# Kernel tuning notes

Measured on AMD Instinct MI355X. Metric: run time of the kernel, lower is better.

The kernel has to match this reference:

```python
import jax, jax.numpy as jnp
import numpy as np
import math

B, S, D, H = 2, 2048, 1024, 16
DH = D // H
DFF = 4 * D
EPS = 1e-6


def layer_norm(x, g, b):
    # Faithful to the torch module: std is Bessel-corrected (ddof=1) and eps is
    # added to std (not variance).
    mean = jnp.mean(x, axis=-1, keepdims=True)
    var = jnp.sum((x - mean) ** 2, axis=-1, keepdims=True) / (x.shape[-1] - 1)
    return g * (x - mean) / (jnp.sqrt(var) + EPS) + b


def gelu_tanh(h):
    c = math.sqrt(2.0 / math.pi)
    return 0.5 * h * (1.0 + jnp.tanh(c * (h + 0.044715 * h ** 3)))


def attention(x, mask, wq, bq, wk, bk, wv, bv, wo, bo):
    b, s, d = x.shape
    q = (x @ wq + bq).reshape(b, s, H, DH)
    k = (x @ wk + bk).reshape(b, s, H, DH)
    v = (x @ wv + bv).reshape(b, s, H, DH)
    corr = jnp.einsum('bqhd,bkhd->bhqk', q, k) / math.sqrt(DH)  # [B,H,S,S]
    # original builds mask[:,None,:].repeat -> key-axis padding mask
    corr = jnp.where(mask[:, None, None, :] == 0, jnp.float32(-1e9), corr)
    prob = jax.nn.softmax(corr, axis=-1)
    hid = jnp.einsum('bhqk,bkhd->bqhd', prob, v).reshape(b, s, d)
    return hid @ wo + bo


def setup_inputs() -> dict:
    key = jax.random.key(0)
    ks = jax.random.split(key, 16)
    std = 0.02
    inp = {
        'hidden': jax.random.normal(ks[0], (B, S, D), jnp.float32),
        'mask': jax.random.randint(ks[1], (B, S), 0, 2, jnp.int32),
        'wq': jax.random.normal(ks[2], (D, D), jnp.float32) * std,
        'bq': jnp.zeros((D,), jnp.float32),
        'wk': jax.random.normal(ks[3], (D, D), jnp.float32) * std,
        'bk': jnp.zeros((D,), jnp.float32),
        'wv': jax.random.normal(ks[4], (D, D), jnp.float32) * std,
        'bv': jnp.zeros((D,), jnp.float32),
        'wo': jax.random.normal(ks[5], (D, D), jnp.float32) * std,
        'bo': jnp.zeros((D,), jnp.float32),
        'w1': jax.random.normal(ks[6], (D, DFF), jnp.float32) * std,
        'b1': jnp.zeros((DFF,), jnp.float32),
        'w2': jax.random.normal(ks[7], (DFF, D), jnp.float32) * std,
        'b2': jnp.zeros((D,), jnp.float32),
        'ln1_g': jnp.ones((D,), jnp.float32),
        'ln1_b': jnp.zeros((D,), jnp.float32),
        'ln2_g': jnp.ones((D,), jnp.float32),
        'ln2_b': jnp.zeros((D,), jnp.float32),
    }
    return inp


def reference(hidden, mask, wq, bq, wk, bk, wv, bv, wo, bo, w1, b1, w2, b2,
              ln1_g, ln1_b, ln2_g, ln2_b):
    # pre-norm residual attention sublayer (dropout = identity in eval)
    h = hidden + attention(layer_norm(hidden, ln1_g, ln1_b), mask,
                           wq, bq, wk, bk, wv, bv, wo, bo)
    # pre-norm residual FFN sublayer with tanh-GELU
    ff_in = layer_norm(h, ln2_g, ln2_b)
    h = h + (gelu_tanh(ff_in @ w1 + b1) @ w2 + b2)
    return h
```

## Files before the change

### kernel.cpp

```cpp
#include <hip/hip_runtime.h>

#define BB 2
#define SS 2048
#define DD 1024
#define HH 16
#define DHH 64
#define DFF 4096
#define MM (BB * SS)

typedef unsigned short u16;
typedef short short8 __attribute__((ext_vector_type(8)));
typedef float f32x4 __attribute__((ext_vector_type(4)));

__device__ __forceinline__ float b2f(u16 u) {
    return __uint_as_float(((unsigned)u) << 16);
}
__device__ __forceinline__ u16 f2b(float f) {
    unsigned u = __float_as_uint(f);
    unsigned r = (u + 0x7fffu + ((u >> 16) & 1u)) >> 16;
    return (u16)r;
}
__device__ __forceinline__ float gelu_tanh_f(float x) {
    float x3 = x * x * x;
    float t = 0.7978845608028654f * (x + 0.044715f * x3);
    return 0.5f * x * (1.0f + tanhf(t));
}
__device__ __forceinline__ void cp16(const u16* g, u16* l) {
    __builtin_amdgcn_global_load_lds(
        (const __attribute__((address_space(1))) void*)g,
        (__attribute__((address_space(3))) void*)l, 16, 0, 0);
}

__global__ __launch_bounds__(256) void wconv(const float* __restrict__ W,
                                             u16* __restrict__ WT,
                                             int Kdim, int Ndim) {
    __shared__ float tile[64][65];
    const int t = threadIdx.x;
    const int k0 = blockIdx.x * 64, n0 = blockIdx.y * 64;
    const int c = t & 63, r0 = (t >> 6) * 16;
#pragma unroll
    for (int i = 0; i < 16; ++i)
        tile[r0 + i][c] = W[(size_t)(k0 + r0 + i) * Ndim + n0 + c];
    __syncthreads();
    const int k4 = (t & 15) * 4, nr = t >> 4;
#pragma unroll
    for (int i = 0; i < 4; ++i) {
        int n = nr + 16 * i;
        ushort4 u = {f2b(tile[k4 + 0][n]), f2b(tile[k4 + 1][n]),
                     f2b(tile[k4 + 2][n]), f2b(tile[k4 + 3][n])};
        *(ushort4*)&WT[(size_t)(n0 + n) * Kdim + k0 + k4] = u;
    }
}

__global__ __launch_bounds__(256) void pack3(const float* __restrict__ a,
                                             const float* __restrict__ b,
                                             const float* __restrict__ c,
                                             float* __restrict__ o) {
    int i = blockIdx.x * 256 + threadIdx.x;
    o[i] = (i < 1024) ? a[i] : ((i < 2048) ? b[i - 1024] : c[i - 2048]);
}

template <typename TI>
__global__ __launch_bounds__(256) void ln_kernel(const TI* __restrict__ x,
                                                 const float* __restrict__ g,
                                                 const float* __restrict__ bb,
                                                 u16* __restrict__ out) {
    __shared__ float red[8];
    const int row = blockIdx.x;
    const int t = threadIdx.x;
    const size_t base = (size_t)row * DD;

    float xv[4];
#pragma unroll
    for (int i = 0; i < 4; ++i) {
        int j = t + i * 256;
        if constexpr (sizeof(TI) == 2) xv[i] = b2f(((const u16*)x)[base + j]);
        else                            xv[i] = ((const float*)x)[base + j];
    }

    float part = xv[0] + xv[1] + xv[2] + xv[3];
#pragma unroll
    for (int off = 32; off > 0; off >>= 1) part += __shfl_xor(part, off);
    if ((t & 63) == 0) red[t >> 6] = part;
    __syncthreads();
    const float mean = (red[0] + red[1] + red[2] + red[3]) * (1.0f / 1024.0f);

    float dv[4];
#pragma unroll
    for (int i = 0; i < 4; ++i) dv[i] = xv[i] - mean;
    float p2 = dv[0] * dv[0] + dv[1] * dv[1] + dv[2] * dv[2] + dv[3] * dv[3];
#pragma unroll
    for (int off = 32; off > 0; off >>= 1) p2 += __shfl_xor(p2, off);
    if ((t & 63) == 0) red[4 + (t >> 6)] = p2;
    __syncthreads();
    const float var = (red[4] + red[5] + red[6] + red[7]) * (1.0f / 1023.0f);
    const float rden = 1.0f / (sqrtf(var) + 1e-6f);

#pragma unroll
    for (int i = 0; i < 4; ++i) {
        int j = t + i * 256;
        out[base + j] = f2b(g[j] * dv[i] * rden + bb[j]);
    }
}

template <int EPI>
__device__ __forceinline__ void gemm_store(int row, int col, float v,
                                           const void* res, void* out, int Ndim) {
    if (EPI == 0 || EPI == 4) {
        if (EPI == 4) v *= 0.125f;
        const int bq = row >> 11, ss = row & 2047;
        const int hh = col >> 6, dh = col & 63;
        ((u16*)out)[(((size_t)bq * HH + hh) * SS + ss) * DHH + dh] = f2b(v);
    } else if (EPI == 5) {
        const int reg = col >> 10, cc = col & 1023;
        if (reg == 0) v *= 0.125f;
        const int bq = row >> 11, ss = row & 2047;
        const int hh = cc >> 6, dh = cc & 63;
        ((u16*)out)[(size_t)reg * 4194304 +
                    (((size_t)bq * HH + hh) * SS + ss) * DHH + dh] = f2b(v);
    } else if (EPI == 1) {
        const size_t o = (size_t)row * Ndim + col;
        ((u16*)out)[o] = f2b(v + ((const float*)res)[o]);
    } else if (EPI == 2) {
        ((u16*)out)[(size_t)row * Ndim + col] = f2b(gelu_tanh_f(v));
    } else {
        const size_t o = (size_t)row * Ndim + col;
        ((float*)out)[o] = v + b2f(((const u16*)res)[o]);
    }
}

template <int EPI, int TM>
__global__ __launch_bounds__(256) void gemm_as(const u16* __restrict__ A,
                                               const u16* __restrict__ BTg,
                                               const float* __restrict__ bias,
                                               const void* __restrict__ res,
                                               void* __restrict__ out,
                                               int Ndim, int Kdim) {
    constexpr int NI = (TM == 128) ? 4 : 2;
    constexpr int NCA = TM / 32;
    __shared__ __align__(16) u16 As[TM * 64];
    __shared__ __align__(16) u16 Bs[128 * 64];

    const int t = threadIdx.x;
    const int w = t >> 6, l = t & 63;
    const int lm = l & 15, lg = l >> 4;
    const int m0 = blockIdx.y * TM, n0 = blockIdx.x * 128;
    const int wro = (TM == 128) ? (w >> 1) * 64 : 0;
    const int wco = (TM == 128) ? (w & 1) * 64 : w * 32;

    f32x4 acc[4][NI];
#pragma unroll
    for (int mi = 0; mi < 4; ++mi)
#pragma unroll
        for (int ni = 0; ni < NI; ++ni) acc[mi][ni] = (f32x4){0.f, 0.f, 0.f, 0.f};

    for (int k0 = 0; k0 < Kdim; k0 += 64) {
#pragma unroll
        for (int j = 0; j < NCA; ++j) {
            const int c = (w * NCA + j) * 64 + l;
            const int r = c >> 3, g = (c & 7) ^ (r & 7);
            cp16(A + (size_t)(m0 + r) * Kdim + k0 + g * 8,
                 &As[(w * NCA + j) * 512]);
        }
#pragma unroll
        for (int j = 0; j < 4; ++j) {
            const int c = (w * 4 + j) * 64 + l;
            const int r = c >> 3, g = (c & 7) ^ (r & 7);
            cp16(BTg + (size_t)(n0 + r) * Kdim + k0 + g * 8,
                 &Bs[(w * 4 + j) * 512]);
        }
        __syncthreads();

#pragma unroll
        for (int ks = 0; ks < 64; ks += 32) {
            short8 af[4], bf[NI];
#pragma unroll
            for (int mi = 0; mi < 4; ++mi) {
                const int row = wro + mi * 16 + lm;
                af[mi] = *(const short8*)&As[row * 64 + ((ks + lg * 8) ^ ((row & 7) * 8))];
            }
#pragma unroll
            for (int ni = 0; ni < NI; ++ni) {
                const int nn = wco + ni * 16 + lm;
                bf[ni] = *(const short8*)&Bs[nn * 64 + ((ks + lg * 8) ^ ((nn & 7) * 8))];
            }
#pragma unroll
            for (int mi = 0; mi < 4; ++mi)
#pragma unroll
                for (int ni = 0; ni < NI; ++ni)
                    acc[mi][ni] = __builtin_amdgcn_mfma_f32_16x16x32_bf16(
                        af[mi], bf[ni], acc[mi][ni], 0, 0, 0);
        }
        __syncthreads();
    }

#pragma unroll
    for (int ni = 0; ni < NI; ++ni) {
        const int col = n0 + wco + ni * 16 + lm;
        const float bv = bias[col];
#pragma unroll
        for (int mi = 0; mi < 4; ++mi)
#pragma unroll
            for (int r = 0; r < 4; ++r)
                gemm_store<EPI>(m0 + wro + mi * 16 + lg * 4 + r, col,
                                acc[mi][ni][r] + bv, res, out, Ndim);
    }
}

template <int EPI, int TM>
__global__ __launch_bounds__(256) void gemm_fb(const u16* __restrict__ A,
                                               const float* __restrict__ W,
                                               const float* __restrict__ bias,
                                               const void* __restrict__ res,
                                               void* __restrict__ out,
                                               int Ndim, int Kdim) {
    constexpr int NI = (TM == 128) ? 4 : 2;
    __shared__ __align__(16) u16 As[TM * 64];
    __shared__ __align__(16) u16 BT[128 * 64];

    const int t = threadIdx.x;
    const int w = t >> 6, l = t & 63;
    const int lm = l & 15, lg = l >> 4;
    const int m0 = blockIdx.y * TM, n0 = blockIdx.x * 128;
    const int wro = (TM == 128) ? (w >> 1) * 64 : 0;
    const int wco = (TM == 128) ? (w & 1) * 64 : w * 32;

    f32x4 acc[4][NI];
#pragma unroll
    for (int mi = 0; mi < 4; ++mi)
#pragma unroll
        for (int ni = 0; ni < NI; ++ni) acc[mi][ni] = (f32x4){0.f, 0.f, 0.f, 0.f};

    const int bn = t & 127;
    const int bk4 = (t >> 7) * 4;

    for (int k0 = 0; k0 < Kdim; k0 += 64) {
#pragma unroll
        for (int it = 0; it < TM / 32; ++it) {
            int idx = it * 256 + t;
            int row = idx >> 3, c8 = (idx & 7) * 8;
            short8 v = *(const short8*)(A + (size_t)(m0 + row) * Kdim + k0 + c8);
            *(short8*)&As[row * 64 + (c8 ^ ((row & 7) * 8))] = v;
        }
#pragma unroll
        for (int it = 0; it < 8; ++it) {
            int kq = it * 8 + bk4;
            const float* wp = W + (size_t)(k0 + kq) * Ndim + n0 + bn;
            ushort4 u = {f2b(wp[0]), f2b(wp[(size_t)Ndim]),
                         f2b(wp[2 * (size_t)Ndim]), f2b(wp[3 * (size_t)Ndim])};
            *(ushort4*)&BT[bn * 64 + (kq ^ ((bn & 7) * 8))] = u;
        }
        __syncthreads();

#pragma unroll
        for (int ks = 0; ks < 64; ks += 32) {
            short8 af[4], bf[NI];
#pragma unroll
            for (int mi = 0; mi < 4; ++mi) {
                const int row = wro + mi * 16 + lm;
                af[mi] = *(const short8*)&As[row * 64 + ((ks + lg * 8) ^ ((row & 7) * 8))];
            }
#pragma unroll
            for (int ni = 0; ni < NI; ++ni) {
                const int nn = wco + ni * 16 + lm;
                bf[ni] = *(const short8*)&BT[nn * 64 + ((ks + lg * 8) ^ ((nn & 7) * 8))];
            }
#pragma unroll
            for (int mi = 0; mi < 4; ++mi)
#pragma unroll
                for (int ni = 0; ni < NI; ++ni)
                    acc[mi][ni] = __builtin_amdgcn_mfma_f32_16x16x32_bf16(
                        af[mi], bf[ni], acc[mi][ni], 0, 0, 0);
        }
        __syncthreads();
    }

#pragma unroll
    for (int ni = 0; ni < NI; ++ni) {
        const int col = n0 + wco + ni * 16 + lm;
        const float bv = bias[col];
#pragma unroll
        for (int mi = 0; mi < 4; ++mi)
#pragma unroll
            for (int r = 0; r < 4; ++r)
                gemm_store<EPI>(m0 + wro + mi * 16 + lg * 4 + r, col,
                                acc[mi][ni][r] + bv, res, out, Ndim);
    }
}

__global__ __launch_bounds__(256) void attn_mfma2(const u16* __restrict__ qg,
                                                  const u16* __restrict__ kg,
                                                  const u16* __restrict__ vg,
                                                  const int* __restrict__ mask,
                                                  u16* __restrict__ hid) {
    __shared__ __align__(16) u16 Ks[64 * 72];
    __shared__ __align__(16) u16 VTs[64 * 72];
    __shared__ __align__(16) float maskf[64];

    const int t = threadIdx.x;
    const int w = t >> 6;
    const int l = t & 63;
    const int lm = l & 15, lg = l >> 4;
    const int h = blockIdx.y, b = blockIdx.z;
    const int qbase = blockIdx.x * 128 + w * 32;
    const size_t bhS = ((size_t)b * HH + h) * SS;

    short8 qlo[2], qhi[2];
#pragma unroll
    for (int qp = 0; qp < 2; ++qp) {
        const u16* qrow = qg + (bhS + qbase + qp * 16 + lm) * DHH + lg * 8;
        qlo[qp] = *(const short8*)qrow;
        qhi[qp] = *(const short8*)(qrow + 32);
    }

    f32x4 acc[2][4];
#pragma unroll
    for (int qp = 0; qp < 2; ++qp)
#pragma unroll
        for (int i = 0; i < 4; ++i) acc[qp][i] = (f32x4){0.f, 0.f, 0.f, 0.f};
    float sume[2] = {0.f, 0.f};

    const int kq = (t & 15) * 4, dq = (t >> 4) * 4;

    for (int kt = 0; kt < SS; kt += 64) {
        __syncthreads();
#pragma unroll
        for (int it = 0; it < 4; ++it) {
            int idx = it * 256 + t;
            int row = idx >> 4, c4 = (idx & 15) * 4;
            ushort4 u = *(const ushort4*)(kg + (bhS + kt + row) * DHH + c4);
            *(ushort4*)&Ks[row * 72 + c4] = u;
        }
        {
            ushort4 a0 = *(const ushort4*)(vg + (bhS + kt + kq + 0) * DHH + dq);
            ushort4 a1 = *(const ushort4*)(vg + (bhS + kt + kq + 1) * DHH + dq);
            ushort4 a2 = *(const ushort4*)(vg + (bhS + kt + kq + 2) * DHH + dq);
            ushort4 a3 = *(const ushort4*)(vg + (bhS + kt + kq + 3) * DHH + dq);
            ushort4 w0 = {a0.x, a1.x, a2.x, a3.x};
            ushort4 w1 = {a0.y, a1.y, a2.y, a3.y};
            ushort4 w2 = {a0.z, a1.z, a2.z, a3.z};
            ushort4 w3 = {a0.w, a1.w, a2.w, a3.w};
            *(ushort4*)&VTs[(dq + 0) * 72 + kq] = w0;
            *(ushort4*)&VTs[(dq + 1) * 72 + kq] = w1;
            *(ushort4*)&VTs[(dq + 2) * 72 + kq] = w2;
            *(ushort4*)&VTs[(dq + 3) * 72 + kq] = w3;
        }
        if (t < 64) maskf[t] = mask[b * SS + kt + t] ? 1.0f : 0.0f;
        __syncthreads();

#pragma unroll
        for (int kb = 0; kb < 64; kb += 32) {
            short8 kfa[2], kfc[2];
#pragma unroll
            for (int s = 0; s < 2; ++s) {
                const int keyrow = kb + 8 * (lm >> 2) + 4 * s + (lm & 3);
                const u16* kr = &Ks[keyrow * 72 + lg * 8];
                kfa[s] = *(const short8*)kr;
                kfc[s] = *(const short8*)(kr + 32);
            }
            short8 p8[2];
#pragma unroll
            for (int qp = 0; qp < 2; ++qp) {
                float ev[8];
#pragma unroll
                for (int s = 0; s < 2; ++s) {
                    f32x4 c = (f32x4){0.f, 0.f, 0.f, 0.f};
                    c = __builtin_amdgcn_mfma_f32_16x16x32_bf16(kfa[s], qlo[qp], c, 0, 0, 0);
                    c = __builtin_amdgcn_mfma_f32_16x16x32_bf16(kfc[s], qhi[qp], c, 0, 0, 0);
                    const float4 mv = *(const float4*)&maskf[kb + 8 * lg + 4 * s];
                    float e0 = __expf(c[0]) * mv.x;
                    float e1 = __expf(c[1]) * mv.y;
                    float e2 = __expf(c[2]) * mv.z;
                    float e3 = __expf(c[3]) * mv.w;
                    sume[qp] += e0 + e1 + e2 + e3;
                    ev[4 * s + 0] = e0; ev[4 * s + 1] = e1;
                    ev[4 * s + 2] = e2; ev[4 * s + 3] = e3;
                }
#pragma unroll
                for (int i = 0; i < 8; ++i)
                    p8[qp][i] = (short)(__float_as_uint(ev[i]) >> 16);
            }
#pragma unroll
            for (int d0 = 0; d0 < 4; ++d0) {
                const short8 v8 = *(const short8*)&VTs[(d0 * 16 + lm) * 72 + kb + lg * 8];
#pragma unroll
                for (int qp = 0; qp < 2; ++qp)
                    acc[qp][d0] = __builtin_amdgcn_mfma_f32_16x16x32_bf16(
                        p8[qp], v8, acc[qp][d0], 0, 0, 0);
            }
        }
    }

#pragma unroll
    for (int qp = 0; qp < 2; ++qp) {
        float s = sume[qp];
        s += __shfl_xor(s, 16);
        s += __shfl_xor(s, 32);
        float rinv[4];
#pragma unroll
        for (int r = 0; r < 4; ++r) rinv[r] = 1.0f / __shfl(s, 4 * lg + r);
#pragma unroll
        for (int d0 = 0; d0 < 4; ++d0)
#pragma unroll
            for (int r = 0; r < 4; ++r) {
                const int q = qbase + qp * 16 + 4 * lg + r;
                hid[(size_t)(b * SS + q) * DD + h * DHH + d0 * 16 + lm] =
                    f2b(acc[qp][d0][r] * rinv[r]);
            }
    }
}

extern "C" void kernel_launch(void* const* d_in, const int* in_sizes, int n_in,
                              void* d_out, int out_size, void* d_ws, size_t ws_size,
                              hipStream_t stream) {
    (void)in_sizes; (void)n_in; (void)out_size;

    const float* hidden = (const float*)d_in[0];
    const int*   mask   = (const int*)d_in[1];
    const float* wq = (const float*)d_in[2];  const float* bq = (const float*)d_in[3];
    const float* wk = (const float*)d_in[4];  const float* bk = (const float*)d_in[5];
    const float* wv = (const float*)d_in[6];  const float* bv = (const float*)d_in[7];
    const float* wo = (const float*)d_in[8];  const float* bo = (const float*)d_in[9];
    const float* w1 = (const float*)d_in[10]; const float* b1 = (const float*)d_in[11];
    const float* w2 = (const float*)d_in[12]; const float* b2 = (const float*)d_in[13];
    const float* ln1g = (const float*)d_in[14]; const float* ln1b = (const float*)d_in[15];
    const float* ln2g = (const float*)d_in[16]; const float* ln2b = (const float*)d_in[17];

    char* ws = (char*)d_ws;
    u16* R0 = (u16*)(ws + 0);
    u16* R1 = (u16*)(ws + 8388608);
    u16* R2 = (u16*)(ws + 16777216);
    u16* R3 = (u16*)(ws + 25165824);
    float* outp = (float*)d_out;

    const size_t WTOFF = 33554432;
    const bool big = ws_size >= WTOFF + 25165824 + 16384;

    if (big) {
        u16* qkvT = (u16*)(ws + WTOFF);
        u16* woT  = (u16*)(ws + WTOFF + 6291456);
        u16* w1T  = (u16*)(ws + WTOFF + 8388608);
        u16* w2T  = (u16*)(ws + WTOFF + 16777216);
        float* bqkv = (float*)(ws + WTOFF + 25165824);

        wconv<<<dim3(DD / 64, DD / 64), 256, 0, stream>>>(wq, qkvT, DD, DD);
        wconv<<<dim3(DD / 64, DD / 64), 256, 0, stream>>>(wk, qkvT + (size_t)1024 * DD, DD, DD);
        wconv<<<dim3(DD / 64, DD / 64), 256, 0, stream>>>(wv, qkvT + (size_t)2048 * DD, DD, DD);
        wconv<<<dim3(DD / 64, DD / 64), 256, 0, stream>>>(wo, woT, DD, DD);
        wconv<<<dim3(DD / 64, DFF / 64), 256, 0, stream>>>(w1, w1T, DD, DFF);
        wconv<<<dim3(DFF / 64, DD / 64), 256, 0, stream>>>(w2, w2T, DFF, DD);
        pack3<<<12, 256, 0, stream>>>(bq, bk, bv, bqkv);

        ln_kernel<float><<<MM, 256, 0, stream>>>(hidden, ln1g, ln1b, R0);
        gemm_as<5, 128><<<dim3(3072 / 128, MM / 128), 256, 0, stream>>>(
            R0, qkvT, bqkv, nullptr, R1, 3072, DD);
        attn_mfma2<<<dim3(SS / 128, HH, BB), 256, 0, stream>>>(R1, R2, R3, mask, R0);
        gemm_as<1, 128><<<dim3(DD / 128, MM / 128), 256, 0, stream>>>(
            R0, woT, bo, hidden, R3, DD, DD);
        ln_kernel<u16><<<MM, 256, 0, stream>>>(R3, ln2g, ln2b, R0);
        for (int s2 = 0; s2 < 2; ++s2) {
            const size_t r0 = (size_t)s2 * 2048;
            gemm_as<2, 128><<<dim3(DFF / 128, 2048 / 128), 256, 0, stream>>>(
                R0 + r0 * DD, w1T, b1, nullptr, R1, DFF, DD);
            gemm_as<3, 64><<<dim3(DD / 128, 2048 / 64), 256, 0, stream>>>(
                R1, w2T, b2, R3 + r0 * DD, outp + r0 * DD, DD, DFF);
        }
    } else {
        ln_kernel<float><<<MM, 256, 0, stream>>>(hidden, ln1g, ln1b, R0);
        gemm_fb<4, 128><<<dim3(DD / 128, MM / 128), 256, 0, stream>>>(R0, wq, bq, nullptr, R1, DD, DD);
        gemm_fb<0, 128><<<dim3(DD / 128, MM / 128), 256, 0, stream>>>(R0, wk, bk, nullptr, R2, DD, DD);
        gemm_fb<0, 128><<<dim3(DD / 128, MM / 128), 256, 0, stream>>>(R0, wv, bv, nullptr, R3, DD, DD);
        attn_mfma2<<<dim3(SS / 128, HH, BB), 256, 0, stream>>>(R1, R2, R3, mask, R0);
        gemm_fb<1, 128><<<dim3(DD / 128, MM / 128), 256, 0, stream>>>(R0, wo, bo, hidden, R3, DD, DD);
        ln_kernel<u16><<<MM, 256, 0, stream>>>(R3, ln2g, ln2b, R0);
        for (int s2 = 0; s2 < 2; ++s2) {
            const size_t r0 = (size_t)s2 * 2048;
            gemm_fb<2, 128><<<dim3(DFF / 128, 2048 / 128), 256, 0, stream>>>(
                R0 + r0 * DD, w1, b1, nullptr, R1, DFF, DD);
            gemm_fb<3, 64><<<dim3(DD / 128, 2048 / 64), 256, 0, stream>>>(
                R1, w2, b2, R3 + r0 * DD, outp + r0 * DD, DD, DFF);
        }
    }
}
```

Measured before the change: 491.3 us.

## Split attention over key halves with merge kernel, batch weight conversions

Attention is split along the key dimension into two halves, doubling the grid so more workgroups can fill the GPU. Each half writes unnormalized bf16 partial outputs and per-row exp sums, and a new merge kernel adds the two partials and divides by the total sum. The six weight-conversion launches are merged into two kernels, and the second one runs after attention so its output buffer can hold the attention partials first. This adds extra global traffic for the partials, an extra bf16 rounding of the unnormalized values, and reuses the output buffer as scratch space.

```diff
diff --git a/kernel.cpp b/kernel.cpp
--- a/kernel.cpp
+++ b/kernel.cpp
@@ -31,12 +31,11 @@
         (__attribute__((address_space(3))) void*)l, 16, 0, 0);
 }
 
-__global__ __launch_bounds__(256) void wconv(const float* __restrict__ W,
-                                             u16* __restrict__ WT,
-                                             int Kdim, int Ndim) {
-    __shared__ float tile[64][65];
-    const int t = threadIdx.x;
-    const int k0 = blockIdx.x * 64, n0 = blockIdx.y * 64;
+__device__ __forceinline__ void wconv_tile(const float* __restrict__ W,
+                                           u16* __restrict__ WT,
+                                           int Kdim, int Ndim, int gk, int gn,
+                                           float (*tile)[65], int t) {
+    const int k0 = gk * 64, n0 = gn * 64;
     const int c = t & 63, r0 = (t >> 6) * 16;
 #pragma unroll
     for (int i = 0; i < 16; ++i)
@@ -49,6 +48,38 @@
         ushort4 u = {f2b(tile[k4 + 0][n]), f2b(tile[k4 + 1][n]),
                      f2b(tile[k4 + 2][n]), f2b(tile[k4 + 3][n])};
         *(ushort4*)&WT[(size_t)(n0 + n) * Kdim + k0 + k4] = u;
+    }
+}
+
+__global__ __launch_bounds__(256) void wconvA(const float* __restrict__ wq,
+                                              const float* __restrict__ wk,
+                                              const float* __restrict__ wv,
+                                              const float* __restrict__ w2,
+                                              u16* __restrict__ qkvT,
+                                              u16* __restrict__ w2T) {
+    __shared__ float tile[64][65];
+    const int bid = blockIdx.x, t = threadIdx.x;
+    if (bid < 768) {
+        const int r = bid >> 8, li = bid & 255;
+        const float* W = (r == 0) ? wq : ((r == 1) ? wk : wv);
+        wconv_tile(W, qkvT + (size_t)r * 1048576, DD, DD, li & 15, li >> 4, tile, t);
+    } else {
+        const int li = bid - 768;
+        wconv_tile(w2, w2T, DFF, DD, li & 63, li >> 6, tile, t);
+    }
+}
+
+__global__ __launch_bounds__(256) void wconvB(const float* __restrict__ wo,
+                                              const float* __restrict__ w1,
+                                              u16* __restrict__ woT,
+                                              u16* __restrict__ w1T) {
+    __shared__ float tile[64][65];
+    const int bid = blockIdx.x, t = threadIdx.x;
+    if (bid < 256) {
+        wconv_tile(wo, woT, DD, DD, bid & 15, bid >> 4, tile, t);
+    } else {
+        const int li = bid - 256;
+        wconv_tile(w1, w1T, DD, DFF, li & 15, li >> 4, tile, t);
     }
 }
 
@@ -288,11 +319,13 @@
     }
 }
 
-__global__ __launch_bounds__(256) void attn_mfma2(const u16* __restrict__ qg,
+__global__ __launch_bounds__(256) void attn_split(const u16* __restrict__ qg,
                                                   const u16* __restrict__ kg,
                                                   const u16* __restrict__ vg,
                                                   const int* __restrict__ mask,
-                                                  u16* __restrict__ hid) {
+                                                  u16* __restrict__ p0,
+                                                  u16* __restrict__ p1,
+                                                  float* __restrict__ sume_g) {
     __shared__ __align__(16) u16 Ks[64 * 72];
     __shared__ __align__(16) u16 VTs[64 * 72];
     __shared__ __align__(16) float maskf[64];
@@ -301,9 +334,13 @@
     const int w = t >> 6;
     const int l = t & 63;
     const int lm = l & 15, lg = l >> 4;
-    const int h = blockIdx.y, b = blockIdx.z;
+    const int h = blockIdx.y;
+    const int z = blockIdx.z;
+    const int b = z >> 1, half = z & 1;
     const int qbase = blockIdx.x * 128 + w * 32;
     const size_t bhS = ((size_t)b * HH + h) * SS;
+    u16* pO = half ? p1 : p0;
+    const int kt0 = half * (SS / 2);
 
     short8 qlo[2], qhi[2];
 #pragma unroll
@@ -322,7 +359,7 @@
 
     const int kq = (t & 15) * 4, dq = (t >> 4) * 4;
 
-    for (int kt = 0; kt < SS; kt += 64) {
+    for (int kt = kt0; kt < kt0 + SS / 2; kt += 64) {
         __syncthreads();
 #pragma unroll
         for (int it = 0; it < 4; ++it) {
@@ -396,6 +433,144 @@
         float s = sume[qp];
         s += __shfl_xor(s, 16);
         s += __shfl_xor(s, 32);
+        if (l < 16)
+            sume_g[(size_t)half * (BB * HH * SS) + bhS + qbase + qp * 16 + lm] = s;
+#pragma unroll
+        for (int d0 = 0; d0 < 4; ++d0)
+#pragma unroll
+            for (int r = 0; r < 4; ++r) {
+                const int q = qbase + qp * 16 + 4 * lg + r;
+                pO[(size_t)(b * SS + q) * DD + h * DHH + d0 * 16 + lm] =
+                    f2b(acc[qp][d0][r]);
+            }
+    }
+}
+
+__global__ __launch_bounds__(256) void attn_merge(const u16* __restrict__ p1,
+                                                  const float* __restrict__ sume_g,
+                                                  u16* __restrict__ hid) {
+    const int row = blockIdx.x;
+    const int b = row >> 11, s = row & 2047;
+    const int t = threadIdx.x;
+#pragma unroll
+    for (int i = 0; i < 4; ++i) {
+        const int j = t + i * 256;
+        const int h = j >> 6;
+        const size_t si = ((size_t)b * HH + h) * SS + s;
+        const float d = sume_g[si] + sume_g[(size_t)BB * HH * SS + si];
+        const size_t o = (size_t)row * DD + j;
+        hid[o] = f2b((b2f(hid[o]) + b2f(p1[o])) / d);
+    }
+}
+
+__global__ __launch_bounds__(256) void attn_mfma2(const u16* __restrict__ qg,
+                                                  const u16* __restrict__ kg,
+                                                  const u16* __restrict__ vg,
+                                                  const int* __restrict__ mask,
+                                                  u16* __restrict__ hid) {
+    __shared__ __align__(16) u16 Ks[64 * 72];
+    __shared__ __align__(16) u16 VTs[64 * 72];
+    __shared__ __align__(16) float maskf[64];
+
+    const int t = threadIdx.x;
+    const int w = t >> 6;
+    const int l = t & 63;
+    const int lm = l & 15, lg = l >> 4;
+    const int h = blockIdx.y, b = blockIdx.z;
+    const int qbase = blockIdx.x * 128 + w * 32;
+    const size_t bhS = ((size_t)b * HH + h) * SS;
+
+    short8 qlo[2], qhi[2];
+#pragma unroll
+    for (int qp = 0; qp < 2; ++qp) {
+        const u16* qrow = qg + (bhS + qbase + qp * 16 + lm) * DHH + lg * 8;
+        qlo[qp] = *(const short8*)qrow;
+        qhi[qp] = *(const short8*)(qrow + 32);
+    }
+
+    f32x4 acc[2][4];
+#pragma unroll
+    for (int qp = 0; qp < 2; ++qp)
+#pragma unroll
+        for (int i = 0; i < 4; ++i) acc[qp][i] = (f32x4){0.f, 0.f, 0.f, 0.f};
+    float sume[2] = {0.f, 0.f};
+
+    const int kq = (t & 15) * 4, dq = (t >> 4) * 4;
+
+    for (int kt = 0; kt < SS; kt += 64) {
+        __syncthreads();
+#pragma unroll
+        for (int it = 0; it < 4; ++it) {
+            int idx = it * 256 + t;
+            int row = idx >> 4, c4 = (idx & 15) * 4;
+            ushort4 u = *(const ushort4*)(kg + (bhS + kt + row) * DHH + c4);
+            *(ushort4*)&Ks[row * 72 + c4] = u;
+        }
+        {
+            ushort4 a0 = *(const ushort4*)(vg + (bhS + kt + kq + 0) * DHH + dq);
+            ushort4 a1 = *(const ushort4*)(vg + (bhS + kt + kq + 1) * DHH + dq);
+            ushort4 a2 = *(const ushort4*)(vg + (bhS + kt + kq + 2) * DHH + dq);
+            ushort4 a3 = *(const ushort4*)(vg + (bhS + kt + kq + 3) * DHH + dq);
+            ushort4 w0 = {a0.x, a1.x, a2.x, a3.x};
+            ushort4 w1 = {a0.y, a1.y, a2.y, a3.y};
+            ushort4 w2 = {a0.z, a1.z, a2.z, a3.z};
+            ushort4 w3 = {a0.w, a1.w, a2.w, a3.w};
+            *(ushort4*)&VTs[(dq + 0) * 72 + kq] = w0;
+            *(ushort4*)&VTs[(dq + 1) * 72 + kq] = w1;
+            *(ushort4*)&VTs[(dq + 2) * 72 + kq] = w2;
+            *(ushort4*)&VTs[(dq + 3) * 72 + kq] = w3;
+        }
+        if (t < 64) maskf[t] = mask[b * SS + kt + t] ? 1.0f : 0.0f;
+        __syncthreads();
+
+#pragma unroll
+        for (int kb = 0; kb < 64; kb += 32) {
+            short8 kfa[2], kfc[2];
+#pragma unroll
+            for (int s = 0; s < 2; ++s) {
+                const int keyrow = kb + 8 * (lm >> 2) + 4 * s + (lm & 3);
+                const u16* kr = &Ks[keyrow * 72 + lg * 8];
+                kfa[s] = *(const short8*)kr;
+                kfc[s] = *(const short8*)(kr + 32);
+            }
+            short8 p8[2];
+#pragma unroll
+            for (int qp = 0; qp < 2; ++qp) {
+                float ev[8];
+#pragma unroll
+                for (int s = 0; s < 2; ++s) {
+                    f32x4 c = (f32x4){0.f, 0.f, 0.f, 0.f};
+                    c = __builtin_amdgcn_mfma_f32_16x16x32_bf16(kfa[s], qlo[qp], c, 0, 0, 0);
+                    c = __builtin_amdgcn_mfma_f32_16x16x32_bf16(kfc[s], qhi[qp], c, 0, 0, 0);
+                    const float4 mv = *(const float4*)&maskf[kb + 8 * lg + 4 * s];
+                    float e0 = __expf(c[0]) * mv.x;
+                    float e1 = __expf(c[1]) * mv.y;
+                    float e2 = __expf(c[2]) * mv.z;
+                    float e3 = __expf(c[3]) * mv.w;
+                    sume[qp] += e0 + e1 + e2 + e3;
+                    ev[4 * s + 0] = e0; ev[4 * s + 1] = e1;
+                    ev[4 * s + 2] = e2; ev[4 * s + 3] = e3;
+                }
+#pragma unroll
+                for (int i = 0; i < 8; ++i)
+                    p8[qp][i] = (short)(__float_as_uint(ev[i]) >> 16);
+            }
+#pragma unroll
+            for (int d0 = 0; d0 < 4; ++d0) {
+                const short8 v8 = *(const short8*)&VTs[(d0 * 16 + lm) * 72 + kb + lg * 8];
+#pragma unroll
+                for (int qp = 0; qp < 2; ++qp)
+                    acc[qp][d0] = __builtin_amdgcn_mfma_f32_16x16x32_bf16(
+                        p8[qp], v8, acc[qp][d0], 0, 0, 0);
+            }
+        }
+    }
+
+#pragma unroll
+    for (int qp = 0; qp < 2; ++qp) {
+        float s = sume[qp];
+        s += __shfl_xor(s, 16);
+        s += __shfl_xor(s, 32);
         float rinv[4];
 #pragma unroll
         for (int r = 0; r < 4; ++r) rinv[r] = 1.0f / __shfl(s, 4 * lg + r);
@@ -442,19 +617,19 @@
         u16* w1T  = (u16*)(ws + WTOFF + 8388608);
         u16* w2T  = (u16*)(ws + WTOFF + 16777216);
         float* bqkv = (float*)(ws + WTOFF + 25165824);
-
-        wconv<<<dim3(DD / 64, DD / 64), 256, 0, stream>>>(wq, qkvT, DD, DD);
-        wconv<<<dim3(DD / 64, DD / 64), 256, 0, stream>>>(wk, qkvT + (size_t)1024 * DD, DD, DD);
-        wconv<<<dim3(DD / 64, DD / 64), 256, 0, stream>>>(wv, qkvT + (size_t)2048 * DD, DD, DD);
-        wconv<<<dim3(DD / 64, DD / 64), 256, 0, stream>>>(wo, woT, DD, DD);
-        wconv<<<dim3(DD / 64, DFF / 64), 256, 0, stream>>>(w1, w1T, DD, DFF);
-        wconv<<<dim3(DFF / 64, DD / 64), 256, 0, stream>>>(w2, w2T, DFF, DD);
+        u16* p1 = w1T;
+        float* sume_g = (float*)d_out;
+
+        wconvA<<<1792, 256, 0, stream>>>(wq, wk, wv, w2, qkvT, w2T);
         pack3<<<12, 256, 0, stream>>>(bq, bk, bv, bqkv);
 
         ln_kernel<float><<<MM, 256, 0, stream>>>(hidden, ln1g, ln1b, R0);
         gemm_as<5, 128><<<dim3(3072 / 128, MM / 128), 256, 0, stream>>>(
             R0, qkvT, bqkv, nullptr, R1, 3072, DD);
-        attn_mfma2<<<dim3(SS / 128, HH, BB), 256, 0, stream>>>(R1, R2, R3, mask, R0);
+        attn_split<<<dim3(SS / 128, HH, BB * 2), 256, 0, stream>>>(
+            R1, R2, R3, mask, R0, p1, sume_g);
+        attn_merge<<<MM, 256, 0, stream>>>(p1, sume_g, R0);
+        wconvB<<<1280, 256, 0, stream>>>(wo, w1, woT, w1T);
         gemm_as<1, 128><<<dim3(DD / 128, MM / 128), 256, 0, stream>>>(
             R0, woT, bo, hidden, R3, DD, DD);
         ln_kernel<u16><<<MM, 256, 0, stream>>>(R3, ln2g, ln2b, R0);
```

Measured after the change: 492.9 us. No clear change (+0.3%).
